# Kernel optimization log

Hardware: AMD Instinct MI355X
Metric: run time of the kernel (lower is better)

Reference implementation:

```python
import jax, jax.numpy as jnp
import numpy as np

B, S, D = 1, 4096, 1024
H, DH = 8, 128
SCALING = 256.0 ** -0.5
SOFTCAP = 50.0
WINDOW = 512
EPS = 1e-6
NEG = -1e30


def setup_inputs() -> dict:
    key = jax.random.key(0)
    ks = jax.random.split(key, 8)
    hidden_states = jax.random.normal(ks[0], (B, S, D), dtype=jnp.float32)
    # rope tables: plausible cos/sin in [-1,1]
    inv_freq = 1.0 / (10000.0 ** (jnp.arange(0, DH, 2, dtype=jnp.float32) / DH))
    t = jnp.arange(S, dtype=jnp.float32)
    freqs = jnp.outer(t, inv_freq)  # [S, DH/2]
    emb = jnp.concatenate([freqs, freqs], axis=-1)  # [S, DH]
    cos = jnp.cos(emb)[None]  # [1, S, DH]
    sin = jnp.sin(emb)[None]
    w = 0.02
    Wq = jax.random.normal(ks[1], (H * DH, D), dtype=jnp.float32) * w
    Wk = jax.random.normal(ks[2], (H * DH, D), dtype=jnp.float32) * w
    Wv = jax.random.normal(ks[3], (H * DH, D), dtype=jnp.float32) * w
    Wo = jax.random.normal(ks[4], (D, H * DH), dtype=jnp.float32) * w
    q_norm_w = jnp.zeros((DH,), dtype=jnp.float32)
    k_norm_w = jnp.zeros((DH,), dtype=jnp.float32)
    return {"hidden_states": hidden_states, "cos": cos, "sin": sin,
            "Wq": Wq, "Wk": Wk, "Wv": Wv, "Wo": Wo,
            "q_norm_w": q_norm_w, "k_norm_w": k_norm_w}


def _rms_norm(x, w):
    # Gemma3 RMSNorm: x * rsqrt(mean(x^2) + eps) * (1 + w)
    var = jnp.mean(jnp.square(x), axis=-1, keepdims=True)
    return x * jax.lax.rsqrt(var + EPS) * (1.0 + w)


def _rotate_half(x):
    x1, x2 = jnp.split(x, 2, axis=-1)
    return jnp.concatenate([-x2, x1], axis=-1)


def reference(hidden_states, cos, sin, Wq, Wk, Wv, Wo, q_norm_w, k_norm_w):
    b, s, _ = hidden_states.shape
    # QKV projections -> [B, H, S, DH]
    q = (hidden_states @ Wq.T).reshape(b, s, H, DH).transpose(0, 2, 1, 3)
    k = (hidden_states @ Wk.T).reshape(b, s, H, DH).transpose(0, 2, 1, 3)
    v = (hidden_states @ Wv.T).reshape(b, s, H, DH).transpose(0, 2, 1, 3)
    # per-head RMSNorm on q and k
    q = _rms_norm(q, q_norm_w)
    k = _rms_norm(k, k_norm_w)
    # RoPE (cos/sin broadcast over heads via unsqueeze(1))
    c = cos[:, None, :, :]
    si = sin[:, None, :, :]
    q = q * c + _rotate_half(q) * si
    k = k * c + _rotate_half(k) * si
    # scores with scaling and logit softcapping
    scores = jnp.einsum('bhqd,bhkd->bhqk', q, k) * SCALING
    scores = SOFTCAP * jnp.tanh(scores / SOFTCAP)
    # causal + sliding-window mask: attend to j with 0 <= i - j < WINDOW (plus j == i)
    i = jnp.arange(s)[:, None]
    j = jnp.arange(s)[None, :]
    mask = (j <= i) & (i - j < WINDOW)  # [S, S]
    scores = jnp.where(mask[None, None], scores, NEG)
    probs = jax.nn.softmax(scores, axis=-1)  # [B, H, S, S]
    attn = jnp.einsum('bhqk,bhkd->bhqd', probs, v)
    attn = attn.transpose(0, 2, 1, 3).reshape(b, s, H * DH)
    out = attn @ Wo.T
    return out, probs
```

## Files before the change

kernel.cpp:

```cpp
#include <hip/hip_runtime.h>

#define S_LEN 4096

typedef _Float16 f16;
typedef __bf16 bf16;
typedef __attribute__((ext_vector_type(4))) _Float16 f16x4;
typedef __attribute__((ext_vector_type(8))) _Float16 f16x8;
typedef __attribute__((ext_vector_type(8))) __bf16 bf16x8;
typedef __attribute__((ext_vector_type(4))) float f32x4;

__device__ __forceinline__ void async_cp16(void* lds, const void* g) {
  __builtin_amdgcn_global_load_lds((const __attribute__((address_space(1))) void*)g,
                                   (__attribute__((address_space(3))) void*)lds, 16, 0, 0);
}

__device__ __forceinline__ f32x4 mfma16(f16x8 a, f16x8 b, f32x4 c) {
  return __builtin_amdgcn_mfma_f32_16x16x32_f16(a, b, c, 0, 0, 0);
}

__global__ void detect_dtype(const unsigned short* __restrict__ x, int* __restrict__ flag) {
  const int t = threadIdx.x;
  int cnt = 0;
  for (int i = t; i < 16384; i += 256) {
    const int e = (x[i] >> 7) & 0xFF;
    cnt += (e >= 0x87);
  }
#pragma unroll
  for (int m = 1; m < 64; m <<= 1) cnt += __shfl_xor(cnt, m);
  __shared__ int red[4];
  if ((t & 63) == 0) red[t >> 6] = cnt;
  __syncthreads();
  if (t == 0) *flag = (red[0] + red[1] + red[2] + red[3] > 64) ? 1 : 0;
}

__global__ void cvt_f16(const void* __restrict__ src, f16* __restrict__ dst, int n,
                        const int* __restrict__ flagp) {
  const int i = (blockIdx.x * 256 + threadIdx.x) * 8;
  if (i >= n) return;
  f16x8 o;
  if (*flagp) {
    const float* s = (const float*)src;
#pragma unroll
    for (int j = 0; j < 8; ++j) o[j] = (f16)s[i + j];
  } else {
    const bf16x8 v = *(const bf16x8*)((const bf16*)src + i);
#pragma unroll
    for (int j = 0; j < 8; ++j) o[j] = (f16)(float)v[j];
  }
  *(f16x8*)(dst + i) = o;
}

__global__ void cvt_w4(const void* __restrict__ s0, const void* __restrict__ s1,
                       const void* __restrict__ s2, const void* __restrict__ s3,
                       f16* __restrict__ wqkv, f16* __restrict__ woh,
                       const int* __restrict__ flagp) {
  const int b = blockIdx.x >> 9;
  const int i = ((blockIdx.x & 511) * 256 + threadIdx.x) * 8;
  const void* src = (b == 0) ? s0 : (b == 1) ? s1 : (b == 2) ? s2 : s3;
  f16* dst = (b < 3) ? (wqkv + (size_t)b * 1048576) : woh;
  f16x8 o;
  if (*flagp) {
    const float* s = (const float*)src;
#pragma unroll
    for (int j = 0; j < 8; ++j) o[j] = (f16)s[i + j];
  } else {
    const bf16x8 v = *(const bf16x8*)((const bf16*)src + i);
#pragma unroll
    for (int j = 0; j < 8; ++j) o[j] = (f16)(float)v[j];
  }
  *(f16x8*)(dst + i) = o;
}

__global__ void cvt_misc(const void* __restrict__ c, const void* __restrict__ s,
                         const void* __restrict__ qn, const void* __restrict__ kn,
                         float* __restrict__ cd, float* __restrict__ sd,
                         float* __restrict__ qnd, float* __restrict__ knd,
                         const int* __restrict__ flagp) {
  const int fp = *flagp;
  const int b = blockIdx.x;
  if (b < 4096) {
    const void* src = (b < 2048) ? c : s;
    float* dst = (b < 2048) ? cd : sd;
    const int i = (b & 2047) * 256 + threadIdx.x;
    dst[i] = fp ? ((const float*)src)[i] : (float)((const bf16*)src)[i];
  } else {
    const int t = threadIdx.x;
    if (t < 128) qnd[t] = fp ? ((const float*)qn)[t] : (float)((const bf16*)qn)[t];
    else knd[t - 128] = fp ? ((const float*)kn)[t - 128] : (float)((const bf16*)kn)[t - 128];
  }
}

template <int MODE>
__launch_bounds__(256, 1)
__global__ void gemm128(const f16* __restrict__ A, const f16* __restrict__ B,
                        void* __restrict__ Cv, int K, int N, const int* __restrict__ flagp) {
  __shared__ f16 As[128 * 64];
  __shared__ f16 Bs[128 * 64];
  const int tid = threadIdx.x;
  const int w = tid >> 6, l = tid & 63;
  const int n0 = blockIdx.x * 128, m0 = blockIdx.y * 128;
  const int wm = (w >> 1) * 64, wn = (w & 1) * 64;
  const int fp = flagp ? *flagp : 0;
  f32x4 acc[4][4] = {};
  for (int k0 = 0; k0 < K; k0 += 64) {
#pragma unroll
    for (int it = 0; it < 4; ++it) {
      const int c = it * 4 + w;
      const int row = c * 8 + (l >> 3);
      const int dq = (l & 7) ^ (row & 7);
      async_cp16(&As[c * 512], &A[(size_t)(m0 + row) * K + k0 + dq * 8]);
      async_cp16(&Bs[c * 512], &B[(size_t)(n0 + row) * K + k0 + dq * 8]);
    }
    __syncthreads();
#pragma unroll
    for (int ks = 0; ks < 2; ++ks) {
      f16x8 af[4], bfr[4];
#pragma unroll
      for (int i = 0; i < 4; ++i) {
        const int ra = wm + i * 16 + (l & 15);
        af[i] = *(const f16x8*)&As[ra * 64 + (((ks * 4 + (l >> 4)) ^ (ra & 7)) << 3)];
        const int rb = wn + i * 16 + (l & 15);
        bfr[i] = *(const f16x8*)&Bs[rb * 64 + (((ks * 4 + (l >> 4)) ^ (rb & 7)) << 3)];
      }
#pragma unroll
      for (int mi = 0; mi < 4; ++mi)
#pragma unroll
        for (int ni = 0; ni < 4; ++ni)
          acc[mi][ni] = mfma16(af[mi], bfr[ni], acc[mi][ni]);
    }
    __syncthreads();
  }
#pragma unroll
  for (int mi = 0; mi < 4; ++mi)
#pragma unroll
    for (int ni = 0; ni < 4; ++ni) {
      const int col = n0 + wn + ni * 16 + (l & 15);
      const int row = m0 + wm + mi * 16 + ((l >> 4) << 2);
#pragma unroll
      for (int r = 0; r < 4; ++r) {
        const size_t off = (size_t)(row + r) * N + col;
        if (MODE == 1)      ((f16*)Cv)[off] = (f16)acc[mi][ni][r];
        else if (fp)        ((float*)Cv)[off] = acc[mi][ni][r];
        else                ((bf16*)Cv)[off] = (bf16)acc[mi][ni][r];
      }
    }
}

__global__ void rope_rms2(const f16* __restrict__ QKV, const float* __restrict__ cosp,
                          const float* __restrict__ sinp, const float* __restrict__ qnw,
                          const float* __restrict__ knw, f16* __restrict__ qh,
                          f16* __restrict__ kh) {
  const int w = threadIdx.x >> 6, l = threadIdx.x & 63;
  const int p = blockIdx.x * 4 + w;
  const int s = p >> 3, h = p & 7;
  const int part = blockIdx.y;
  const float* nw = part ? knw : qnw;
  f16* outb = part ? kh : qh;
  const f16* xr = QKV + (size_t)s * 3072 + part * 1024 + h * 128;
  const float x0 = (float)xr[l], x1 = (float)xr[l + 64];
  float ss = x0 * x0 + x1 * x1;
#pragma unroll
  for (int m = 1; m < 64; m <<= 1) ss += __shfl_xor(ss, m);
  const float r = rsqrtf(ss * (1.f / 128.f) + 1e-6f);
  const float g0 = r * (1.f + nw[l]);
  const float g1 = r * (1.f + nw[l + 64]);
  const float c0 = cosp[s * 128 + l], c1 = cosp[s * 128 + l + 64];
  const float s0 = sinp[s * 128 + l], s1 = sinp[s * 128 + l + 64];
  const float xn0 = x0 * g0, xn1 = x1 * g1;
  f16* o = outb + ((size_t)h * S_LEN + s) * 128;
  o[l] = (f16)(xn0 * c0 - xn1 * s0);
  o[l + 64] = (f16)(xn1 * c1 + xn0 * s1);
}

__global__ void vtrans(const f16* __restrict__ vh, f16* __restrict__ vt) {
  __shared__ f16 tle[64][65];
  const int s0 = blockIdx.x * 64, n0 = blockIdx.y * 64;
  const int tid = threadIdx.x;
#pragma unroll
  for (int i = 0; i < 16; ++i) {
    const int idx = i * 256 + tid;
    tle[idx >> 6][idx & 63] = vh[(size_t)(s0 + (idx >> 6)) * 3072 + 2048 + n0 + (idx & 63)];
  }
  __syncthreads();
  const int h = n0 >> 7, dh0 = n0 & 127;
#pragma unroll
  for (int i = 0; i < 16; ++i) {
    const int idx = i * 256 + tid;
    vt[((size_t)h * 128 + dh0 + (idx >> 6)) * S_LEN + s0 + (idx & 63)] = tle[idx & 63][idx >> 6];
  }
}

__launch_bounds__(256, 2)
__global__ void attn64(const f16* __restrict__ Qh, const f16* __restrict__ Kh,
                       const f16* __restrict__ Vt, f16* __restrict__ Pc,
                       void* __restrict__ dout, f16* __restrict__ Oh,
                       const int* __restrict__ flagp) {
  __shared__ f16 Qs[64 * 128];
  __shared__ f16 Ks[64 * 128];
  __shared__ f16 Vs[128 * 64];
  const int tid = threadIdx.x, w = tid >> 6, l = tid & 63;
  const int q0 = blockIdx.x * 64, h = blockIdx.y;
  const int kt0 = (q0 >= 512) ? ((q0 - 511) >> 6) : 0;
  const int kt1 = (q0 + 64) >> 6;
  const int fp = *flagp;

#pragma unroll
  for (int it = 0; it < 4; ++it) {
    const int c = it * 4 + w;
    const int row = c * 4 + (l >> 4);
    const int dq = (l & 15) ^ (row & 15);
    async_cp16(&Qs[c * 512], &Qh[((size_t)h * S_LEN + q0 + row) * 128 + dq * 8]);
  }
  __syncthreads();
  f16x8 qfrag[4];
#pragma unroll
  for (int ks = 0; ks < 4; ++ks) {
    const int r = w * 16 + (l & 15);
    qfrag[ks] = *(const f16x8*)&Qs[r * 128 + (((ks * 4 + (l >> 4)) ^ (r & 15)) << 3)];
  }
  __syncthreads();

  f16* Ps = Qs + w * 1024;
  float* Ls = (float*)(Qs + 4096);
  float l_i[4] = {0.f, 0.f, 0.f, 0.f};
  f32x4 oacc[8] = {};

  for (int t = kt0; t < kt1; ++t) {
#pragma unroll
    for (int it = 0; it < 4; ++it) {
      const int c = it * 4 + w;
      { const int row = c * 4 + (l >> 4);
        const int dq = (l & 15) ^ (row & 15);
        async_cp16(&Ks[c * 512], &Kh[((size_t)h * S_LEN + t * 64 + row) * 128 + dq * 8]); }
      { const int row = c * 8 + (l >> 3);
        const int dq = (l & 7) ^ (row & 7);
        async_cp16(&Vs[c * 512], &Vt[((size_t)h * 128 + row) * S_LEN + t * 64 + dq * 8]); }
    }
    __syncthreads();
    f32x4 sacc[4] = {};
#pragma unroll
    for (int ks = 0; ks < 4; ++ks) {
      f16x8 kfrag[4];
#pragma unroll
      for (int ni = 0; ni < 4; ++ni) {
        const int r = ni * 16 + (l & 15);
        kfrag[ni] = *(const f16x8*)&Ks[r * 128 + (((ks * 4 + (l >> 4)) ^ (r & 15)) << 3)];
      }
#pragma unroll
      for (int ni = 0; ni < 4; ++ni)
        sacc[ni] = mfma16(qfrag[ks], kfrag[ni], sacc[ni]);
    }
#pragma unroll
    for (int reg = 0; reg < 4; ++reg) {
      const int pr = ((l >> 4) << 2) + reg;
      const int q = q0 + w * 16 + pr;
      float rs = 0.f;
#pragma unroll
      for (int ni = 0; ni < 4; ++ni) {
        const int col = t * 64 + ni * 16 + (l & 15);
        float s = sacc[ni][reg] * 0.0625f;
        const float z = __expf(s * 0.04f);
        s = 50.f * (1.f - 2.f / (z + 1.f));
        const bool valid = (col <= q) && (q - col < 512);
        const float p = valid ? __expf(s - 8.f) : 0.f;
        rs += p;
        const int pc = ni * 16 + (l & 15);
        Ps[pr * 64 + (((pc >> 3) ^ (pr & 7)) << 3) + (pc & 7)] = (f16)p;
      }
#pragma unroll
      for (int m = 1; m < 16; m <<= 1) rs += __shfl_xor(rs, m);
      l_i[reg] += rs;
    }
#pragma unroll
    for (int ks = 0; ks < 2; ++ks) {
      const int rp = l & 15;
      const f16x8 pf = *(const f16x8*)&Ps[rp * 64 + (((ks * 4 + (l >> 4)) ^ (rp & 7)) << 3)];
      f16x8 vf[8];
#pragma unroll
      for (int ni = 0; ni < 8; ++ni) {
        const int r = ni * 16 + (l & 15);
        vf[ni] = *(const f16x8*)&Vs[r * 64 + (((ks * 4 + (l >> 4)) ^ (r & 7)) << 3)];
      }
#pragma unroll
      for (int ni = 0; ni < 8; ++ni)
        oacc[ni] = mfma16(pf, vf[ni], oacc[ni]);
    }
    {
      const size_t rowbase = (size_t)h * 4096 + q0 + w * 16;
#pragma unroll
      for (int i = 0; i < 4; ++i) {
        const int pr = i * 4 + (l >> 4);
        const int pc = (l & 15) * 4;
        const f16x4 v = *(const f16x4*)&Ps[pr * 64 + (((pc >> 3) ^ (pr & 7)) << 3) + (pc & 7)];
        *(f16x4*)&Pc[(rowbase + pr) * 576 + (t - kt0) * 64 + pc] = v;
      }
    }
    __syncthreads();
  }

  float il[4];
#pragma unroll
  for (int r = 0; r < 4; ++r) il[r] = 1.f / l_i[r];
  if ((l & 15) == 0) {
#pragma unroll
    for (int r = 0; r < 4; ++r) Ls[w * 16 + ((l >> 4) << 2) + r] = il[r];
  }
#pragma unroll
  for (int ni = 0; ni < 8; ++ni) {
    const int row = q0 + w * 16 + ((l >> 4) << 2);
    const int col = h * 128 + ni * 16 + (l & 15);
#pragma unroll
    for (int r = 0; r < 4; ++r)
      Oh[(size_t)(row + r) * 1024 + col] = (f16)(oacc[ni][r] * il[r]);
  }
  __syncthreads();

  const int jc0 = kt0 * 64;
  const int W = (kt1 - kt0) * 64;
  if (fp) {
    float* pb = (float*)dout + 4194304 + (size_t)h * S_LEN * S_LEN;
    for (int u = tid; u < 64 * 1024; u += 256) {
      const int row = u >> 10;
      const int c4 = (u & 1023) << 2;
      f32x4 v = {};
      if (c4 >= jc0 && c4 < jc0 + W) {
        const float sc = Ls[row];
        const f16x4 pv = *(const f16x4*)&Pc[((size_t)h * 4096 + q0 + row) * 576 + (c4 - jc0)];
#pragma unroll
        for (int k = 0; k < 4; ++k) v[k] = (float)pv[k] * sc;
      }
      *(f32x4*)&pb[(size_t)(q0 + row) * S_LEN + c4] = v;
    }
  } else {
    bf16* pb = (bf16*)dout + 4194304 + (size_t)h * S_LEN * S_LEN;
    for (int u = tid; u < 64 * 512; u += 256) {
      const int row = u >> 9;
      const int c8 = (u & 511) << 3;
      bf16x8 v = {};
      if (c8 >= jc0 && c8 < jc0 + W) {
        const float sc = Ls[row];
        const f16x8 pv = *(const f16x8*)&Pc[((size_t)h * 4096 + q0 + row) * 576 + (c8 - jc0)];
#pragma unroll
        for (int k = 0; k < 8; ++k) v[k] = (bf16)((float)pv[k] * sc);
      }
      *(bf16x8*)&pb[(size_t)(q0 + row) * S_LEN + c8] = v;
    }
  }
}

extern "C" void kernel_launch(void* const* d_in, const int* in_sizes, int n_in,
                              void* d_out, int out_size, void* d_ws, size_t ws_size,
                              hipStream_t stream) {
  (void)in_sizes; (void)n_in; (void)out_size; (void)ws_size;
  char* ws = (char*)d_ws;
  f16*   Pc    = (f16*)(ws);
  f16*   qkv   = (f16*)(ws);
  f16*   qh    = (f16*)(ws + (36u << 20));
  f16*   kh    = (f16*)(ws + (44u << 20));
  f16*   vt    = (f16*)(ws + (52u << 20));
  f16*   attnh = (f16*)(ws + (60u << 20));
  f16*   woh   = (f16*)(ws + (68u << 20));
  f16*   hsf   = (f16*)(ws + (70u << 20));
  f16*   wqkv  = (f16*)(ws + (78u << 20));
  float* cosf  = (float*)(ws + (84u << 20));
  float* sinf  = (float*)(ws + (86u << 20));
  float* qnwf  = (float*)(ws + (88u << 20));
  float* knwf  = (float*)(ws + (88u << 20) + 512);
  int*   flag  = (int*)(ws + (88u << 20) + 1024);

  detect_dtype<<<1, 256, 0, stream>>>((const unsigned short*)d_in[0], flag);
  cvt_f16<<<2048, 256, 0, stream>>>(d_in[0], hsf, 4194304, flag);
  cvt_w4<<<2048, 256, 0, stream>>>(d_in[3], d_in[4], d_in[5], d_in[6], wqkv, woh, flag);
  cvt_misc<<<4097, 256, 0, stream>>>(d_in[1], d_in[2], d_in[7], d_in[8],
                                     cosf, sinf, qnwf, knwf, flag);

  gemm128<1><<<dim3(24, 32), 256, 0, stream>>>(hsf, wqkv, qkv, 1024, 3072, flag);
  rope_rms2<<<dim3(8192, 2), 256, 0, stream>>>(qkv, cosf, sinf, qnwf, knwf, qh, kh);
  vtrans<<<dim3(64, 16), 256, 0, stream>>>(qkv, vt);
  attn64<<<dim3(64, 8), 256, 0, stream>>>(qh, kh, vt, Pc, d_out, attnh, flag);
  gemm128<3><<<dim3(8, 32), 256, 0, stream>>>(attnh, woh, d_out, 1024, 1024, flag);
}
```

Before: 729.1 us.

## Double-buffer K/V in attention, split probs write into separate kernel, fuse conversions

Merges the three input conversion kernels into a single launch. In the attention kernel, K/V tiles are now double-buffered so the next tile's async loads are issued before the current tile's compute, which removes the per-iteration load-and-wait. The dense probability matrix write-out (mostly zeros) moves out of the attention kernel into a separate grid-stride kernel with 4096 blocks, so that large store stream spreads across the whole GPU instead of the 512 attention blocks. The cost is extra LDS per attention block, which may reduce occupancy, plus a global buffer of inverse row sums and one more kernel launch.

```diff
diff --git a/kernel.cpp b/kernel.cpp
--- a/kernel.cpp
+++ b/kernel.cpp
@@ -33,12 +33,9 @@
   if (t == 0) *flag = (red[0] + red[1] + red[2] + red[3] > 64) ? 1 : 0;
 }
 
-__global__ void cvt_f16(const void* __restrict__ src, f16* __restrict__ dst, int n,
-                        const int* __restrict__ flagp) {
-  const int i = (blockIdx.x * 256 + threadIdx.x) * 8;
-  if (i >= n) return;
+__device__ __forceinline__ void cvt8(const void* src, f16* dst, int i, int fp) {
   f16x8 o;
-  if (*flagp) {
+  if (fp) {
     const float* s = (const float*)src;
 #pragma unroll
     for (int j = 0; j < 8; ++j) o[j] = (f16)s[i + j];
@@ -50,43 +47,35 @@
   *(f16x8*)(dst + i) = o;
 }
 
-__global__ void cvt_w4(const void* __restrict__ s0, const void* __restrict__ s1,
-                       const void* __restrict__ s2, const void* __restrict__ s3,
-                       f16* __restrict__ wqkv, f16* __restrict__ woh,
-                       const int* __restrict__ flagp) {
-  const int b = blockIdx.x >> 9;
-  const int i = ((blockIdx.x & 511) * 256 + threadIdx.x) * 8;
-  const void* src = (b == 0) ? s0 : (b == 1) ? s1 : (b == 2) ? s2 : s3;
-  f16* dst = (b < 3) ? (wqkv + (size_t)b * 1048576) : woh;
-  f16x8 o;
-  if (*flagp) {
-    const float* s = (const float*)src;
-#pragma unroll
-    for (int j = 0; j < 8; ++j) o[j] = (f16)s[i + j];
-  } else {
-    const bf16x8 v = *(const bf16x8*)((const bf16*)src + i);
-#pragma unroll
-    for (int j = 0; j < 8; ++j) o[j] = (f16)(float)v[j];
-  }
-  *(f16x8*)(dst + i) = o;
-}
-
-__global__ void cvt_misc(const void* __restrict__ c, const void* __restrict__ s,
-                         const void* __restrict__ qn, const void* __restrict__ kn,
-                         float* __restrict__ cd, float* __restrict__ sd,
-                         float* __restrict__ qnd, float* __restrict__ knd,
-                         const int* __restrict__ flagp) {
+__global__ void cvt_all(const void* __restrict__ hs, const void* __restrict__ wq,
+                        const void* __restrict__ wk, const void* __restrict__ wv,
+                        const void* __restrict__ wo, const void* __restrict__ c,
+                        const void* __restrict__ s, const void* __restrict__ qn,
+                        const void* __restrict__ kn, f16* __restrict__ hsf,
+                        f16* __restrict__ wqkv, f16* __restrict__ woh,
+                        float* __restrict__ cd, float* __restrict__ sd,
+                        float* __restrict__ qnd, float* __restrict__ knd,
+                        const int* __restrict__ flagp) {
   const int fp = *flagp;
-  const int b = blockIdx.x;
-  if (b < 4096) {
-    const void* src = (b < 2048) ? c : s;
-    float* dst = (b < 2048) ? cd : sd;
-    const int i = (b & 2047) * 256 + threadIdx.x;
+  const int b = blockIdx.x, tid = threadIdx.x;
+  if (b < 2048) {
+    cvt8(hs, hsf, (b * 256 + tid) * 8, fp);
+  } else if (b < 4096) {
+    const int bb = b - 2048;
+    const int sub = bb >> 9;
+    const int i = ((bb & 511) * 256 + tid) * 8;
+    const void* src = (sub == 0) ? wq : (sub == 1) ? wk : (sub == 2) ? wv : wo;
+    f16* dst = (sub < 3) ? (wqkv + (size_t)sub * 1048576) : woh;
+    cvt8(src, dst, i, fp);
+  } else if (b < 8192) {
+    const int bb = b - 4096;
+    const void* src = (bb < 2048) ? c : s;
+    float* dst = (bb < 2048) ? cd : sd;
+    const int i = (bb & 2047) * 256 + tid;
     dst[i] = fp ? ((const float*)src)[i] : (float)((const bf16*)src)[i];
   } else {
-    const int t = threadIdx.x;
-    if (t < 128) qnd[t] = fp ? ((const float*)qn)[t] : (float)((const bf16*)qn)[t];
-    else knd[t - 128] = fp ? ((const float*)kn)[t - 128] : (float)((const bf16*)kn)[t - 128];
+    if (tid < 128) qnd[tid] = fp ? ((const float*)qn)[tid] : (float)((const bf16*)qn)[tid];
+    else knd[tid - 128] = fp ? ((const float*)kn)[tid - 128] : (float)((const bf16*)kn)[tid - 128];
   }
 }
 
@@ -193,16 +182,14 @@
 __launch_bounds__(256, 2)
 __global__ void attn64(const f16* __restrict__ Qh, const f16* __restrict__ Kh,
                        const f16* __restrict__ Vt, f16* __restrict__ Pc,
-                       void* __restrict__ dout, f16* __restrict__ Oh,
-                       const int* __restrict__ flagp) {
+                       float* __restrict__ Lsg, f16* __restrict__ Oh) {
   __shared__ f16 Qs[64 * 128];
-  __shared__ f16 Ks[64 * 128];
-  __shared__ f16 Vs[128 * 64];
+  __shared__ f16 Ks[2 * 64 * 128];
+  __shared__ f16 Vs[2 * 128 * 64];
   const int tid = threadIdx.x, w = tid >> 6, l = tid & 63;
   const int q0 = blockIdx.x * 64, h = blockIdx.y;
   const int kt0 = (q0 >= 512) ? ((q0 - 511) >> 6) : 0;
   const int kt1 = (q0 + 64) >> 6;
-  const int fp = *flagp;
 
 #pragma unroll
   for (int it = 0; it < 4; ++it) {
@@ -211,6 +198,16 @@
     const int dq = (l & 15) ^ (row & 15);
     async_cp16(&Qs[c * 512], &Qh[((size_t)h * S_LEN + q0 + row) * 128 + dq * 8]);
   }
+#pragma unroll
+  for (int it = 0; it < 4; ++it) {
+    const int c = it * 4 + w;
+    { const int row = c * 4 + (l >> 4);
+      const int dq = (l & 15) ^ (row & 15);
+      async_cp16(&Ks[c * 512], &Kh[((size_t)h * S_LEN + kt0 * 64 + row) * 128 + dq * 8]); }
+    { const int row = c * 8 + (l >> 3);
+      const int dq = (l & 7) ^ (row & 7);
+      async_cp16(&Vs[c * 512], &Vt[((size_t)h * 128 + row) * S_LEN + kt0 * 64 + dq * 8]); }
+  }
   __syncthreads();
   f16x8 qfrag[4];
 #pragma unroll
@@ -221,22 +218,27 @@
   __syncthreads();
 
   f16* Ps = Qs + w * 1024;
-  float* Ls = (float*)(Qs + 4096);
   float l_i[4] = {0.f, 0.f, 0.f, 0.f};
   f32x4 oacc[8] = {};
 
   for (int t = kt0; t < kt1; ++t) {
-#pragma unroll
-    for (int it = 0; it < 4; ++it) {
-      const int c = it * 4 + w;
-      { const int row = c * 4 + (l >> 4);
-        const int dq = (l & 15) ^ (row & 15);
-        async_cp16(&Ks[c * 512], &Kh[((size_t)h * S_LEN + t * 64 + row) * 128 + dq * 8]); }
-      { const int row = c * 8 + (l >> 3);
-        const int dq = (l & 7) ^ (row & 7);
-        async_cp16(&Vs[c * 512], &Vt[((size_t)h * 128 + row) * S_LEN + t * 64 + dq * 8]); }
-    }
-    __syncthreads();
+    const int cur = (t - kt0) & 1;
+    const int kb = cur * 8192, vb = cur * 8192;
+    if (t + 1 < kt1) {
+      const int nb = (cur ^ 1) * 8192;
+#pragma unroll
+      for (int it = 0; it < 4; ++it) {
+        const int c = it * 4 + w;
+        { const int row = c * 4 + (l >> 4);
+          const int dq = (l & 15) ^ (row & 15);
+          async_cp16(&Ks[nb + c * 512],
+                     &Kh[((size_t)h * S_LEN + (t + 1) * 64 + row) * 128 + dq * 8]); }
+        { const int row = c * 8 + (l >> 3);
+          const int dq = (l & 7) ^ (row & 7);
+          async_cp16(&Vs[nb + c * 512],
+                     &Vt[((size_t)h * 128 + row) * S_LEN + (t + 1) * 64 + dq * 8]); }
+      }
+    }
     f32x4 sacc[4] = {};
 #pragma unroll
     for (int ks = 0; ks < 4; ++ks) {
@@ -244,7 +246,7 @@
 #pragma unroll
       for (int ni = 0; ni < 4; ++ni) {
         const int r = ni * 16 + (l & 15);
-        kfrag[ni] = *(const f16x8*)&Ks[r * 128 + (((ks * 4 + (l >> 4)) ^ (r & 15)) << 3)];
+        kfrag[ni] = *(const f16x8*)&Ks[kb + r * 128 + (((ks * 4 + (l >> 4)) ^ (r & 15)) << 3)];
       }
 #pragma unroll
       for (int ni = 0; ni < 4; ++ni)
@@ -279,7 +281,7 @@
 #pragma unroll
       for (int ni = 0; ni < 8; ++ni) {
         const int r = ni * 16 + (l & 15);
-        vf[ni] = *(const f16x8*)&Vs[r * 64 + (((ks * 4 + (l >> 4)) ^ (r & 7)) << 3)];
+        vf[ni] = *(const f16x8*)&Vs[vb + r * 64 + (((ks * 4 + (l >> 4)) ^ (r & 7)) << 3)];
       }
 #pragma unroll
       for (int ni = 0; ni < 8; ++ni)
@@ -303,7 +305,8 @@
   for (int r = 0; r < 4; ++r) il[r] = 1.f / l_i[r];
   if ((l & 15) == 0) {
 #pragma unroll
-    for (int r = 0; r < 4; ++r) Ls[w * 16 + ((l >> 4) << 2) + r] = il[r];
+    for (int r = 0; r < 4; ++r)
+      Lsg[(h << 12) + q0 + w * 16 + ((l >> 4) << 2) + r] = il[r];
   }
 #pragma unroll
   for (int ni = 0; ni < 8; ++ni) {
@@ -313,37 +316,50 @@
     for (int r = 0; r < 4; ++r)
       Oh[(size_t)(row + r) * 1024 + col] = (f16)(oacc[ni][r] * il[r]);
   }
-  __syncthreads();
-
-  const int jc0 = kt0 * 64;
-  const int W = (kt1 - kt0) * 64;
+}
+
+__launch_bounds__(256)
+__global__ void probs_write(const f16* __restrict__ Pc, const float* __restrict__ Lsg,
+                            void* __restrict__ dout, const int* __restrict__ flagp) {
+  const int fp = *flagp;
+  const long long stride = (long long)gridDim.x * 256;
   if (fp) {
-    float* pb = (float*)dout + 4194304 + (size_t)h * S_LEN * S_LEN;
-    for (int u = tid; u < 64 * 1024; u += 256) {
-      const int row = u >> 10;
-      const int c4 = (u & 1023) << 2;
+    float* pb = (float*)dout + 4194304;
+    const long long total = 8LL * 4096 * 1024;
+    for (long long idx = (long long)blockIdx.x * 256 + threadIdx.x; idx < total; idx += stride) {
+      const int h = (int)(idx >> 22);
+      const int rem = (int)(idx & 4194303);
+      const int row = rem >> 10;
+      const int c = (rem & 1023) << 2;
+      const int q0 = row & ~63;
+      const int jc0 = (q0 >= 512) ? (((q0 - 511) >> 6) << 6) : 0;
       f32x4 v = {};
-      if (c4 >= jc0 && c4 < jc0 + W) {
-        const float sc = Ls[row];
-        const f16x4 pv = *(const f16x4*)&Pc[((size_t)h * 4096 + q0 + row) * 576 + (c4 - jc0)];
+      if (c >= jc0 && c < q0 + 64) {
+        const float sc = Lsg[(h << 12) + row];
+        const f16x4 pv = *(const f16x4*)&Pc[((size_t)(h << 12) + row) * 576 + (c - jc0)];
 #pragma unroll
         for (int k = 0; k < 4; ++k) v[k] = (float)pv[k] * sc;
       }
-      *(f32x4*)&pb[(size_t)(q0 + row) * S_LEN + c4] = v;
+      *(f32x4*)&pb[((size_t)h << 24) + ((size_t)row << 12) + c] = v;
     }
   } else {
-    bf16* pb = (bf16*)dout + 4194304 + (size_t)h * S_LEN * S_LEN;
-    for (int u = tid; u < 64 * 512; u += 256) {
-      const int row = u >> 9;
-      const int c8 = (u & 511) << 3;
+    bf16* pb = (bf16*)dout + 4194304;
+    const long long total = 8LL * 4096 * 512;
+    for (long long idx = (long long)blockIdx.x * 256 + threadIdx.x; idx < total; idx += stride) {
+      const int h = (int)(idx >> 21);
+      const int rem = (int)(idx & 2097151);
+      const int row = rem >> 9;
+      const int c = (rem & 511) << 3;
+      const int q0 = row & ~63;
+      const int jc0 = (q0 >= 512) ? (((q0 - 511) >> 6) << 6) : 0;
       bf16x8 v = {};
-      if (c8 >= jc0 && c8 < jc0 + W) {
-        const float sc = Ls[row];
-        const f16x8 pv = *(const f16x8*)&Pc[((size_t)h * 4096 + q0 + row) * 576 + (c8 - jc0)];
+      if (c >= jc0 && c < q0 + 64) {
+        const float sc = Lsg[(h << 12) + row];
+        const f16x8 pv = *(const f16x8*)&Pc[((size_t)(h << 12) + row) * 576 + (c - jc0)];
 #pragma unroll
         for (int k = 0; k < 8; ++k) v[k] = (bf16)((float)pv[k] * sc);
       }
-      *(bf16x8*)&pb[(size_t)(q0 + row) * S_LEN + c8] = v;
+      *(bf16x8*)&pb[((size_t)h << 24) + ((size_t)row << 12) + c] = v;
     }
   }
 }
@@ -361,6 +377,7 @@
   f16*   attnh = (f16*)(ws + (60u << 20));
   f16*   woh   = (f16*)(ws + (68u << 20));
   f16*   hsf   = (f16*)(ws + (70u << 20));
+  float* Lsg   = (float*)(ws + (70u << 20));
   f16*   wqkv  = (f16*)(ws + (78u << 20));
   float* cosf  = (float*)(ws + (84u << 20));
   float* sinf  = (float*)(ws + (86u << 20));
@@ -369,14 +386,14 @@
   int*   flag  = (int*)(ws + (88u << 20) + 1024);
 
   detect_dtype<<<1, 256, 0, stream>>>((const unsigned short*)d_in[0], flag);
-  cvt_f16<<<2048, 256, 0, stream>>>(d_in[0], hsf, 4194304, flag);
-  cvt_w4<<<2048, 256, 0, stream>>>(d_in[3], d_in[4], d_in[5], d_in[6], wqkv, woh, flag);
-  cvt_misc<<<4097, 256, 0, stream>>>(d_in[1], d_in[2], d_in[7], d_in[8],
-                                     cosf, sinf, qnwf, knwf, flag);
+  cvt_all<<<8193, 256, 0, stream>>>(d_in[0], d_in[3], d_in[4], d_in[5], d_in[6],
+                                    d_in[1], d_in[2], d_in[7], d_in[8],
+                                    hsf, wqkv, woh, cosf, sinf, qnwf, knwf, flag);
 
   gemm128<1><<<dim3(24, 32), 256, 0, stream>>>(hsf, wqkv, qkv, 1024, 3072, flag);
   rope_rms2<<<dim3(8192, 2), 256, 0, stream>>>(qkv, cosf, sinf, qnwf, knwf, qh, kh);
   vtrans<<<dim3(64, 16), 256, 0, stream>>>(qkv, vt);
-  attn64<<<dim3(64, 8), 256, 0, stream>>>(qh, kh, vt, Pc, d_out, attnh, flag);
+  attn64<<<dim3(64, 8), 256, 0, stream>>>(qh, kh, vt, Pc, Lsg, attnh);
+  probs_write<<<4096, 256, 0, stream>>>(Pc, Lsg, d_out, flag);
   gemm128<3><<<dim3(8, 32), 256, 0, stream>>>(attnh, woh, d_out, 1024, 1024, flag);
 }
```

Measured after the change: 727.6 us. About the same (-0.2%).
